# Optimization experiments

Measured on AMD Instinct MI355X. Metric: run time of the kernel, lower is better.

Reference implementation:

```python
import jax, jax.numpy as jnp
import numpy as np

N_JOINTS = 24

def _rodrigues(r):
    # r: [B, J, 3] axis-angle -> [B, J, 3, 3] rotation matrices
    theta = jnp.clip(jnp.linalg.norm(r, axis=-1, keepdims=True), 1e-6)  # [B,J,1]
    rh = r / theta
    z = jnp.zeros_like(rh[..., :1])
    # skew-symmetric matrix m
    m = jnp.stack([
        jnp.concatenate([z, -rh[..., 2:3], rh[..., 1:2]], -1),
        jnp.concatenate([rh[..., 2:3], z, -rh[..., 0:1]], -1),
        jnp.concatenate([-rh[..., 1:2], rh[..., 0:1], z], -1),
    ], axis=-2)  # [B,J,3,3]
    rrT = rh[..., :, None] * rh[..., None, :]  # outer product [B,J,3,3]
    cos = jnp.cos(theta)[..., None]
    sin = jnp.sin(theta)[..., None]
    eye = jnp.eye(3, dtype=r.dtype)
    return cos * eye + (1.0 - cos) * rrT + sin * m

def _with_zeros(Rm, t):
    # Rm: [B,3,3], t: [B,3] -> [B,4,4] homogeneous transform
    B = Rm.shape[0]
    top = jnp.concatenate([Rm, t[:, :, None]], axis=-1)  # [B,3,4]
    bot = jnp.broadcast_to(jnp.array([0.0, 0.0, 0.0, 1.0], Rm.dtype), (B, 1, 4))
    return jnp.concatenate([top, bot], axis=1)

def _keypoints(v, idx):
    # v: [B,N,3], idx: [G,K] vertex-index groups -> [B,G,3] via (max+min)/2
    g = v[:, idx]  # [B,G,K,3] irregular gather
    return (g.max(axis=2) + g.min(axis=2)) * 0.5

def setup_inputs() -> dict:
    key = jax.random.key(0)
    ks = jax.random.split(key, 8)
    B, N, P, K = 64, 40000, 100, 128
    beta = jax.random.normal(ks[0], (B, P), jnp.float32)
    pose = jax.random.normal(ks[1], (B, N_JOINTS * 3), jnp.float32) * 0.3
    trans = jax.random.normal(ks[2], (B, 3), jnp.float32)
    shapedirs = jax.random.normal(ks[3], (P, 3 * N), jnp.float32) * 0.01
    v_template = jax.random.normal(ks[4], (N, 3), jnp.float32)
    w = jax.random.uniform(ks[5], (N, N_JOINTS), jnp.float32)
    weights = w / w.sum(axis=1, keepdims=True)  # LBS weights sum to 1
    reorder_index = jnp.arange(N_JOINTS, dtype=jnp.int64 if jax.config.jax_enable_x64 else jnp.int32)
    # kinematic tree: parent[i] < i (binary-tree shape stands in for the rabbit skeleton)
    parent = jnp.concatenate([jnp.zeros(1, jnp.int32), (jnp.arange(1, N_JOINTS, dtype=jnp.int32) - 1) // 2])
    joint_idx = jax.random.randint(ks[6], (N_JOINTS - 1, K), 0, N)
    add_idx = jax.random.randint(ks[7], (7, K), 0, N)
    return {"beta": beta, "pose": pose, "trans": trans, "shapedirs": shapedirs,
            "v_template": v_template, "weights": weights, "reorder_index": reorder_index,
            "parent": parent, "joint_idx": joint_idx, "add_idx": add_idx}

def reference(beta, pose, trans, shapedirs, v_template, weights,
              reorder_index, parent, joint_idx, add_idx):
    B = beta.shape[0]
    pose = pose.reshape(B, N_JOINTS, 3)[:, reorder_index]
    # blend shapes: v_shaped = beta @ shapedirs + template
    v_posed = (beta @ shapedirs + v_template.reshape(-1)).reshape(B, -1, 3)  # [B,N,3]
    # joints from vertex-group (max+min)/2, root is zero
    J = jnp.concatenate([jnp.zeros((B, 1, 3), beta.dtype), _keypoints(v_posed, joint_idx)], axis=1)  # [B,24,3]
    R = _rodrigues(pose)  # [B,24,3,3]
    # forward kinematics along the tree (fixed 24-joint loop)
    par = np.asarray(jax.device_get(parent))
    G = [_with_zeros(R[:, 0], J[:, 0])]
    for i in range(1, N_JOINTS):
        p = int(par[i])
        G_loc = _with_zeros(R[:, i], J[:, i] - J[:, p])
        G.append(jnp.matmul(G[p], G_loc))
    G = jnp.stack(G, axis=1)  # [B,24,4,4]
    # remove rest-pose joint locations (pack subtraction only touches last column)
    Jh = jnp.concatenate([J, jnp.zeros((B, N_JOINTS, 1), beta.dtype)], axis=-1)[..., None]  # [B,24,4,1]
    t_corr = jnp.matmul(G, Jh)  # [B,24,4,1]
    G1 = jnp.concatenate([G[..., :3], G[..., 3:4] - t_corr], axis=-1)
    # LBS skinning: per-vertex blended transform
    T = jnp.einsum('nk,bkij->bnij', weights, G1)  # [B,N,4,4]
    vh = jnp.concatenate([v_posed, jnp.ones((B, v_posed.shape[1], 1), beta.dtype)], axis=-1)  # [B,N,4]
    posed = jnp.einsum('bnij,bnj->bni', T, vh)[..., :3] + trans[:, None, :]  # [B,N,3]
    skeleton = jnp.concatenate([
        jnp.zeros((B, 1, 3), beta.dtype),
        _keypoints(posed, joint_idx),
        _keypoints(posed, add_idx),
    ], axis=1)  # [B,31,3]
    return posed, skeleton
```

## Files before the change

kernel.cpp:

```cpp
#include <hip/hip_runtime.h>
#include <math.h>

#define B   64
#define NV  40000
#define P   100
#define KG  128
#define NJ  24
#define TV  16
#define NSK 31
#define NSUB (KG / TV)

typedef __attribute__((ext_vector_type(8))) short bf16x8;
typedef __attribute__((ext_vector_type(4))) float f32x4;

__device__ __forceinline__ unsigned short rne_bf16(float f) {
  unsigned u = __float_as_uint(f);
  u = (u + 0x7FFFu + ((u >> 16) & 1u)) >> 16;
  return (unsigned short)u;
}

__global__ __launch_bounds__(256)
void k_jpart(const float* __restrict__ beta,
             const float* __restrict__ sd,
             const float* __restrict__ vt,
             const int*   __restrict__ joint_idx,
             float*       __restrict__ pmn,
             float*       __restrict__ pmx,
             unsigned short* __restrict__ beta_bf) {
  const int j = blockIdx.x;
  const int s = blockIdx.y;
  const int t = threadIdx.x;
  const int lane = t & 63, wv = t >> 6;
  const int l15 = lane & 15, qd = lane >> 4;

  __shared__ __align__(16) unsigned short sdT_s[48 * 136];
  __shared__ __align__(16) float pos_s[64 * 68];
  __shared__ float vt_s[48];
  __shared__ int   idx_s[TV];

  if (t < TV) idx_s[t] = joint_idx[j * KG + s * TV + t];

  if (j == 0 && s == 0) {
    for (int e = t; e < B * 136; e += 256) {
      const int m = e / 136, k = e % 136;
      beta_bf[e] = (k < P) ? rne_bf16(beta[m * P + k]) : (unsigned short)0;
    }
  }
  __syncthreads();

  for (int e = t; e < 48 * 28; e += 256) {
    const int n = e / 28, k = P + e % 28;
    sdT_s[n * 136 + k] = 0;
  }
  for (int task = t; task < TV * P; task += 256) {
    const int v = task / P, k = task % P;
    const float* src = sd + (size_t)k * (3 * NV) + (size_t)idx_s[v] * 3;
    const float f0 = src[0], f1 = src[1], f2 = src[2];
    sdT_s[(v * 3 + 0) * 136 + k] = rne_bf16(f0);
    sdT_s[(v * 3 + 1) * 136 + k] = rne_bf16(f1);
    sdT_s[(v * 3 + 2) * 136 + k] = rne_bf16(f2);
  }
  if (t < 48) vt_s[t] = vt[(size_t)idx_s[t / 3] * 3 + (t % 3)];
  __syncthreads();

  const int m0 = wv * 16 + l15;
  bf16x8 af[4];
#pragma unroll
  for (int ks = 0; ks < 4; ++ks) {
#pragma unroll
    for (int jj = 0; jj < 8; ++jj) {
      const int k = ks * 32 + qd * 8 + jj;
      af[ks][jj] = (short)((k < P) ? rne_bf16(beta[m0 * P + k]) : (unsigned short)0);
    }
  }

  f32x4 acc[3];
#pragma unroll
  for (int nt = 0; nt < 3; ++nt) acc[nt] = (f32x4){0.f, 0.f, 0.f, 0.f};
#pragma unroll
  for (int ks = 0; ks < 4; ++ks) {
#pragma unroll
    for (int nt = 0; nt < 3; ++nt) {
      const bf16x8 bf = *(const bf16x8*)&sdT_s[(nt * 16 + l15) * 136 + ks * 32 + qd * 8];
      acc[nt] = __builtin_amdgcn_mfma_f32_16x16x32_bf16(af[ks], bf, acc[nt], 0, 0, 0);
    }
  }
  float vtv[3];
#pragma unroll
  for (int nt = 0; nt < 3; ++nt) vtv[nt] = vt_s[nt * 16 + l15];

#pragma unroll
  for (int nt = 0; nt < 3; ++nt) {
    const int n = nt * 16 + l15;
    const int v = n / 3, c = n - 3 * v;
#pragma unroll
    for (int r = 0; r < 4; ++r) {
      const int m = wv * 16 + qd * 4 + r;
      pos_s[m * 68 + v * 4 + c] = acc[nt][r] + vtv[nt];
    }
  }
  __syncthreads();

  if (t < 192) {
    const int b = t / 3, c = t % 3;
    float lo = 1e30f, hi = -1e30f;
#pragma unroll
    for (int v = 0; v < TV; ++v) {
      const float val = pos_s[b * 68 + v * 4 + c];
      lo = fminf(lo, val); hi = fmaxf(hi, val);
    }
    pmn[((j * NSUB + s) * B + b) * 3 + c] = lo;
    pmx[((j * NSUB + s) * B + b) * 3 + c] = hi;
  }
}

__global__ void k_chain(const float* __restrict__ pose,
                        const int*   __restrict__ parent,
                        const float* __restrict__ pmn,
                        const float* __restrict__ pmx,
                        const float* __restrict__ trans,
                        unsigned short* __restrict__ G1A) {
  const int b = blockIdx.x;
  const int t = threadIdx.x;

  __shared__ float R[NJ][9];
  __shared__ float Jl[NJ][3];
  __shared__ float G[NJ][12];
  __shared__ float G1c[NJ][12];

  if (t < NJ) {
    const float x = pose[b * NJ * 3 + t * 3 + 0];
    const float y = pose[b * NJ * 3 + t * 3 + 1];
    const float z = pose[b * NJ * 3 + t * 3 + 2];
    const float th = fmaxf(sqrtf(x * x + y * y + z * z), 1e-6f);
    const float xh = x / th, yh = y / th, zh = z / th;
    const float c = cosf(th), s = sinf(th), o = 1.0f - c;
    R[t][0] = c + o * xh * xh;      R[t][1] = o * xh * yh - s * zh; R[t][2] = o * xh * zh + s * yh;
    R[t][3] = o * xh * yh + s * zh; R[t][4] = c + o * yh * yh;      R[t][5] = o * yh * zh - s * xh;
    R[t][6] = o * xh * zh - s * yh; R[t][7] = o * yh * zh + s * xh; R[t][8] = c + o * zh * zh;
    if (t == 0) {
      Jl[0][0] = 0.0f; Jl[0][1] = 0.0f; Jl[0][2] = 0.0f;
    } else {
      const int jj = t - 1;
#pragma unroll
      for (int c2 = 0; c2 < 3; ++c2) {
        float lo = 1e30f, hi = -1e30f;
#pragma unroll
        for (int s2 = 0; s2 < NSUB; ++s2) {
          lo = fminf(lo, pmn[((jj * NSUB + s2) * B + b) * 3 + c2]);
          hi = fmaxf(hi, pmx[((jj * NSUB + s2) * B + b) * 3 + c2]);
        }
        Jl[t][c2] = 0.5f * (lo + hi);
      }
    }
  }
  __syncthreads();

  if (t < 12) {
    const int r = t >> 2, c = t & 3;
    G[0][t] = (c < 3) ? R[0][r * 3 + c] : Jl[0][r];
  }
  __syncthreads();

  for (int i = 1; i < NJ; ++i) {
    const int p = parent[i];
    if (t < 12) {
      const int r = t >> 2, c = t & 3;
      const float g0 = G[p][r * 4 + 0];
      const float g1 = G[p][r * 4 + 1];
      const float g2 = G[p][r * 4 + 2];
      float l0, l1, l2, add;
      if (c < 3) {
        l0 = R[i][0 * 3 + c]; l1 = R[i][1 * 3 + c]; l2 = R[i][2 * 3 + c];
        add = 0.0f;
      } else {
        l0 = Jl[i][0] - Jl[p][0]; l1 = Jl[i][1] - Jl[p][1]; l2 = Jl[i][2] - Jl[p][2];
        add = G[p][r * 4 + 3];
      }
      G[i][t] = g0 * l0 + g1 * l1 + g2 * l2 + add;
    }
    __syncthreads();
  }

  for (int e = t; e < NJ * 12; e += 64) {
    const int i = e / 12, rc = e % 12, r = rc >> 2, c = rc & 3;
    float val;
    if (c < 3) {
      val = G[i][rc];
    } else {
      val = G[i][r * 4 + 3] - (G[i][r * 4 + 0] * Jl[i][0] +
                               G[i][r * 4 + 1] * Jl[i][1] +
                               G[i][r * 4 + 2] * Jl[i][2]);
    }
    G1c[i][rc] = val;
  }
  __syncthreads();

  for (int e = t; e < 512; e += 64) {
    const int m = e >> 5, k = e & 31;
    float val = 0.0f;
    if (m < 12) {
      if (k < NJ) val = G1c[k][m];
      else if (k == NJ && (m & 3) == 3) val = trans[b * 3 + (m >> 2)];
    }
    G1A[(size_t)b * 512 + e] = rne_bf16(val);
  }
}

__global__ __launch_bounds__(256)
void k_skin(const float* __restrict__ sd,
            const float* __restrict__ vt,
            const float* __restrict__ w,
            const unsigned short* __restrict__ beta_bf,
            const unsigned short* __restrict__ G1A,
            float*       __restrict__ out) {
  const int n0v = blockIdx.x * TV;
  const int col0 = n0v * 3;
  const int t  = threadIdx.x;
  const int lane = t & 63, wv = t >> 6;
  const int l15 = lane & 15, q = lane >> 4;

  __shared__ __align__(16) unsigned short sdT_s[48 * 136];
  __shared__ __align__(16) float vhf[64 * 68];

  for (int task = t; task < 768; task += 256) {
    const int n = task % 48, kg = task / 48;
    unsigned pk[4];
#pragma unroll
    for (int h = 0; h < 4; ++h) {
      const int k0 = kg * 8 + 2 * h;
      float f0 = 0.0f, f1 = 0.0f;
      if (k0 < P)     f0 = sd[(size_t)k0 * (3 * NV) + col0 + n];
      if (k0 + 1 < P) f1 = sd[(size_t)(k0 + 1) * (3 * NV) + col0 + n];
      pk[h] = (unsigned)rne_bf16(f0) | ((unsigned)rne_bf16(f1) << 16);
    }
    *(uint4*)&sdT_s[n * 136 + kg * 8] = make_uint4(pk[0], pk[1], pk[2], pk[3]);
  }
  __syncthreads();

  f32x4 acc[3];
#pragma unroll
  for (int nt = 0; nt < 3; ++nt) acc[nt] = (f32x4){0.f, 0.f, 0.f, 0.f};
#pragma unroll
  for (int ks = 0; ks < 4; ++ks) {
    const bf16x8 af = *(const bf16x8*)&beta_bf[(wv * 16 + l15) * 136 + ks * 32 + q * 8];
#pragma unroll
    for (int nt = 0; nt < 3; ++nt) {
      const bf16x8 bf = *(const bf16x8*)&sdT_s[(nt * 16 + l15) * 136 + ks * 32 + q * 8];
      acc[nt] = __builtin_amdgcn_mfma_f32_16x16x32_bf16(af, bf, acc[nt], 0, 0, 0);
    }
  }
  float vtv[3];
#pragma unroll
  for (int nt = 0; nt < 3; ++nt) vtv[nt] = vt[col0 + nt * 16 + l15];

#pragma unroll
  for (int nt = 0; nt < 3; ++nt) {
    const int n = nt * 16 + l15;
    const int v = n / 3, c = n - 3 * v;
#pragma unroll
    for (int r = 0; r < 4; ++r) {
      const int m = wv * 16 + q * 4 + r;
      vhf[m * 68 + v * 4 + c] = acc[nt][r] + vtv[nt];
    }
  }
  __syncthreads();

  bf16x8 wf;
  if (q < 3) {
    const float* wrow = &w[(size_t)(n0v + l15) * NJ + q * 8];
    const float4 w0 = *(const float4*)wrow;
    const float4 w1 = *(const float4*)(wrow + 4);
    wf[0] = (short)rne_bf16(w0.x); wf[1] = (short)rne_bf16(w0.y);
    wf[2] = (short)rne_bf16(w0.z); wf[3] = (short)rne_bf16(w0.w);
    wf[4] = (short)rne_bf16(w1.x); wf[5] = (short)rne_bf16(w1.y);
    wf[6] = (short)rne_bf16(w1.z); wf[7] = (short)rne_bf16(w1.w);
  } else {
    wf = (bf16x8){0, 0, 0, 0, 0, 0, 0, 0};
    wf[0] = (short)0x3F80;
  }
  const f32x4 zero = (f32x4){0.f, 0.f, 0.f, 0.f};
#pragma unroll 4
  for (int bi = 0; bi < 16; ++bi) {
    const int b = wv * 16 + bi;
    const bf16x8 gf = *(const bf16x8*)&G1A[(size_t)b * 512 + l15 * 32 + q * 8];
    const f32x4 d = __builtin_amdgcn_mfma_f32_16x16x32_bf16(gf, wf, zero, 0, 0, 0);
    const float4 vh = *(const float4*)&vhf[b * 68 + l15 * 4];
    if (q < 3) {
      out[(size_t)b * (NV * 3) + col0 + l15 * 3 + q] =
          d[0] * vh.x + d[1] * vh.y + d[2] * vh.z + d[3];
    }
  }
}

__global__ void k_skel(const float* __restrict__ posed,
                       const int*   __restrict__ joint_idx,
                       const int*   __restrict__ add_idx,
                       float*       __restrict__ skel) {
  const int j = blockIdx.x;
  const int b = blockIdx.y;
  const int t = threadIdx.x;
  const int idx = (j < 23) ? joint_idx[j * KG + t] : add_idx[(j - 23) * KG + t];

  const float* p = posed + (size_t)b * NV * 3 + (size_t)idx * 3;
  float mn[3], mx[3];
#pragma unroll
  for (int c = 0; c < 3; ++c) { mn[c] = p[c]; mx[c] = p[c]; }
#pragma unroll
  for (int off = 32; off > 0; off >>= 1) {
#pragma unroll
    for (int c = 0; c < 3; ++c) {
      mn[c] = fminf(mn[c], __shfl_down(mn[c], off));
      mx[c] = fmaxf(mx[c], __shfl_down(mx[c], off));
    }
  }
  __shared__ float s_mn[2][3], s_mx[2][3];
  const int wave = t >> 6, lane = t & 63;
  if (lane == 0) {
#pragma unroll
    for (int c = 0; c < 3; ++c) { s_mn[wave][c] = mn[c]; s_mx[wave][c] = mx[c]; }
  }
  __syncthreads();
  if (t == 0) {
#pragma unroll
    for (int c = 0; c < 3; ++c) {
      float lo = fminf(s_mn[0][c], s_mn[1][c]);
      float hi = fmaxf(s_mx[0][c], s_mx[1][c]);
      skel[(b * NSK + 1 + j) * 3 + c] = 0.5f * (lo + hi);
      if (j == 0) skel[(b * NSK + 0) * 3 + c] = 0.0f;
    }
  }
}

extern "C" void kernel_launch(void* const* d_in, const int* in_sizes, int n_in,
                              void* d_out, int out_size, void* d_ws, size_t ws_size,
                              hipStream_t stream) {
  const float* beta     = (const float*)d_in[0];
  const float* pose     = (const float*)d_in[1];
  const float* trans    = (const float*)d_in[2];
  const float* sd       = (const float*)d_in[3];
  const float* vt       = (const float*)d_in[4];
  const float* w        = (const float*)d_in[5];
  const int* parent     = (const int*)d_in[7];
  const int* joint_idx  = (const int*)d_in[8];
  const int* add_idx    = (const int*)d_in[9];

  float* out = (float*)d_out;
  unsigned short* G1A     = (unsigned short*)d_ws;
  unsigned short* beta_bf = G1A + B * 512;
  float* pmn = (float*)(beta_bf + B * 136);
  float* pmx = pmn + 23 * NSUB * B * 3;

  k_jpart<<<dim3(23, NSUB), 256, 0, stream>>>(beta, sd, vt, joint_idx,
                                              pmn, pmx, beta_bf);
  k_chain<<<B, 64, 0, stream>>>(pose, parent, pmn, pmx, trans, G1A);
  k_skin <<<NV / TV, 256, 0, stream>>>(sd, vt, w, beta_bf, G1A, out);
  k_skel <<<dim3(30, B), 128, 0, stream>>>(out, joint_idx, add_idx,
                                           out + (size_t)B * NV * 3);
}
```

Baseline: 160.7 us.

## Compute skeleton keypoints from gathered vertices instead of re-reading posed output

The skeleton keypoints are now computed by re-skinning only the gathered keypoint vertices, reusing the v_posed tiles that k_jpart already produces (k_jpart now also covers the add_idx groups). The old k_skel kernel did scattered reads of the full posed output after skinning. Beta bf16 conversion moves into a separate prep kernel so k_jpart reads the converted values. This adds two small kernels, extra workspace traffic for the v_posed tiles and more launches, in exchange for removing the dependent scattered gather pass after k_skin.

```diff
diff --git a/kernel.cpp b/kernel.cpp
--- a/kernel.cpp
+++ b/kernel.cpp
@@ -9,6 +9,8 @@
 #define TV  16
 #define NSK 31
 #define NSUB (KG / TV)
+#define NROW 30
+#define VPT  (64 * 68)
 
 typedef __attribute__((ext_vector_type(8))) short bf16x8;
 typedef __attribute__((ext_vector_type(4))) float f32x4;
@@ -19,14 +21,24 @@
   return (unsigned short)u;
 }
 
+__global__ void k_prep(const float* __restrict__ beta,
+                       unsigned short* __restrict__ beta_bf) {
+  const int t = blockIdx.x * 256 + threadIdx.x;
+  if (t < B * 136) {
+    const int m = t / 136, k = t % 136;
+    beta_bf[t] = (k < P) ? rne_bf16(beta[m * P + k]) : (unsigned short)0;
+  }
+}
+
 __global__ __launch_bounds__(256)
-void k_jpart(const float* __restrict__ beta,
+void k_jpart(const unsigned short* __restrict__ beta_bf,
              const float* __restrict__ sd,
              const float* __restrict__ vt,
              const int*   __restrict__ joint_idx,
+             const int*   __restrict__ add_idx,
              float*       __restrict__ pmn,
              float*       __restrict__ pmx,
-             unsigned short* __restrict__ beta_bf) {
+             float*       __restrict__ vposed) {
   const int j = blockIdx.x;
   const int s = blockIdx.y;
   const int t = threadIdx.x;
@@ -38,14 +50,9 @@
   __shared__ float vt_s[48];
   __shared__ int   idx_s[TV];
 
-  if (t < TV) idx_s[t] = joint_idx[j * KG + s * TV + t];
-
-  if (j == 0 && s == 0) {
-    for (int e = t; e < B * 136; e += 256) {
-      const int m = e / 136, k = e % 136;
-      beta_bf[e] = (k < P) ? rne_bf16(beta[m * P + k]) : (unsigned short)0;
-    }
-  }
+  if (t < TV)
+    idx_s[t] = (j < 23) ? joint_idx[j * KG + s * TV + t]
+                        : add_idx[(j - 23) * KG + s * TV + t];
   __syncthreads();
 
   for (int e = t; e < 48 * 28; e += 256) {
@@ -63,26 +70,16 @@
   if (t < 48) vt_s[t] = vt[(size_t)idx_s[t / 3] * 3 + (t % 3)];
   __syncthreads();
 
-  const int m0 = wv * 16 + l15;
-  bf16x8 af[4];
+  f32x4 acc[3];
+#pragma unroll
+  for (int nt = 0; nt < 3; ++nt) acc[nt] = (f32x4){0.f, 0.f, 0.f, 0.f};
 #pragma unroll
   for (int ks = 0; ks < 4; ++ks) {
-#pragma unroll
-    for (int jj = 0; jj < 8; ++jj) {
-      const int k = ks * 32 + qd * 8 + jj;
-      af[ks][jj] = (short)((k < P) ? rne_bf16(beta[m0 * P + k]) : (unsigned short)0);
-    }
-  }
-
-  f32x4 acc[3];
-#pragma unroll
-  for (int nt = 0; nt < 3; ++nt) acc[nt] = (f32x4){0.f, 0.f, 0.f, 0.f};
-#pragma unroll
-  for (int ks = 0; ks < 4; ++ks) {
+    const bf16x8 af = *(const bf16x8*)&beta_bf[(wv * 16 + l15) * 136 + ks * 32 + qd * 8];
 #pragma unroll
     for (int nt = 0; nt < 3; ++nt) {
       const bf16x8 bf = *(const bf16x8*)&sdT_s[(nt * 16 + l15) * 136 + ks * 32 + qd * 8];
-      acc[nt] = __builtin_amdgcn_mfma_f32_16x16x32_bf16(af[ks], bf, acc[nt], 0, 0, 0);
+      acc[nt] = __builtin_amdgcn_mfma_f32_16x16x32_bf16(af, bf, acc[nt], 0, 0, 0);
     }
   }
   float vtv[3];
@@ -101,7 +98,13 @@
   }
   __syncthreads();
 
-  if (t < 192) {
+  {
+    float4* dst = (float4*)(vposed + (size_t)(j * NSUB + s) * VPT);
+    const float4* srcp = (const float4*)pos_s;
+    for (int e = t; e < VPT / 4; e += 256) dst[e] = srcp[e];
+  }
+
+  if (j < 23 && t < 192) {
     const int b = t / 3, c = t % 3;
     float lo = 1e30f, hi = -1e30f;
 #pragma unroll
@@ -208,6 +211,91 @@
 }
 
 __global__ __launch_bounds__(256)
+void k_skel2(const float* __restrict__ vposed,
+             const float* __restrict__ w,
+             const int*   __restrict__ joint_idx,
+             const int*   __restrict__ add_idx,
+             const unsigned short* __restrict__ G1A,
+             float*       __restrict__ pmn2,
+             float*       __restrict__ pmx2) {
+  const int j = blockIdx.x;
+  const int s = blockIdx.y;
+  const int t = threadIdx.x;
+  const int lane = t & 63, wv = t >> 6;
+  const int l15 = lane & 15, q = lane >> 4;
+
+  __shared__ __align__(16) float vhf[64 * 68];
+  __shared__ __align__(16) float pos_s[64 * 68];
+  __shared__ int idx_s[TV];
+
+  if (t < TV)
+    idx_s[t] = (j < 23) ? joint_idx[j * KG + s * TV + t]
+                        : add_idx[(j - 23) * KG + s * TV + t];
+  {
+    const float4* srcp = (const float4*)(vposed + (size_t)(j * NSUB + s) * VPT);
+    float4* dst = (float4*)vhf;
+    for (int e = t; e < VPT / 4; e += 256) dst[e] = srcp[e];
+  }
+  __syncthreads();
+
+  bf16x8 wf;
+  if (q < 3) {
+    const float* wrow = &w[(size_t)idx_s[l15] * NJ + q * 8];
+    const float4 w0 = *(const float4*)wrow;
+    const float4 w1 = *(const float4*)(wrow + 4);
+    wf[0] = (short)rne_bf16(w0.x); wf[1] = (short)rne_bf16(w0.y);
+    wf[2] = (short)rne_bf16(w0.z); wf[3] = (short)rne_bf16(w0.w);
+    wf[4] = (short)rne_bf16(w1.x); wf[5] = (short)rne_bf16(w1.y);
+    wf[6] = (short)rne_bf16(w1.z); wf[7] = (short)rne_bf16(w1.w);
+  } else {
+    wf = (bf16x8){0, 0, 0, 0, 0, 0, 0, 0};
+    wf[0] = (short)0x3F80;
+  }
+  const f32x4 zero = (f32x4){0.f, 0.f, 0.f, 0.f};
+#pragma unroll 4
+  for (int bi = 0; bi < 16; ++bi) {
+    const int b = wv * 16 + bi;
+    const bf16x8 gf = *(const bf16x8*)&G1A[(size_t)b * 512 + l15 * 32 + q * 8];
+    const f32x4 d = __builtin_amdgcn_mfma_f32_16x16x32_bf16(gf, wf, zero, 0, 0, 0);
+    const float4 vh = *(const float4*)&vhf[b * 68 + l15 * 4];
+    if (q < 3) {
+      pos_s[b * 68 + l15 * 4 + q] =
+          d[0] * vh.x + d[1] * vh.y + d[2] * vh.z + d[3];
+    }
+  }
+  __syncthreads();
+
+  if (t < 192) {
+    const int b = t / 3, c = t % 3;
+    float lo = 1e30f, hi = -1e30f;
+#pragma unroll
+    for (int v = 0; v < TV; ++v) {
+      const float val = pos_s[b * 68 + v * 4 + c];
+      lo = fminf(lo, val); hi = fmaxf(hi, val);
+    }
+    pmn2[((j * NSUB + s) * B + b) * 3 + c] = lo;
+    pmx2[((j * NSUB + s) * B + b) * 3 + c] = hi;
+  }
+}
+
+__global__ void k_skelfin(const float* __restrict__ pmn2,
+                          const float* __restrict__ pmx2,
+                          float*       __restrict__ skel) {
+  const int tg = blockIdx.x * 192 + threadIdx.x;
+  const int j = tg / (B * 3);
+  const int rem = tg % (B * 3);
+  const int b = rem / 3, c = rem % 3;
+  float lo = 1e30f, hi = -1e30f;
+#pragma unroll
+  for (int s = 0; s < NSUB; ++s) {
+    lo = fminf(lo, pmn2[((j * NSUB + s) * B + b) * 3 + c]);
+    hi = fmaxf(hi, pmx2[((j * NSUB + s) * B + b) * 3 + c]);
+  }
+  skel[(b * NSK + 1 + j) * 3 + c] = 0.5f * (lo + hi);
+  if (j == 0) skel[(b * NSK + 0) * 3 + c] = 0.0f;
+}
+
+__global__ __launch_bounds__(256)
 void k_skin(const float* __restrict__ sd,
             const float* __restrict__ vt,
             const float* __restrict__ w,
@@ -293,45 +381,6 @@
   }
 }
 
-__global__ void k_skel(const float* __restrict__ posed,
-                       const int*   __restrict__ joint_idx,
-                       const int*   __restrict__ add_idx,
-                       float*       __restrict__ skel) {
-  const int j = blockIdx.x;
-  const int b = blockIdx.y;
-  const int t = threadIdx.x;
-  const int idx = (j < 23) ? joint_idx[j * KG + t] : add_idx[(j - 23) * KG + t];
-
-  const float* p = posed + (size_t)b * NV * 3 + (size_t)idx * 3;
-  float mn[3], mx[3];
-#pragma unroll
-  for (int c = 0; c < 3; ++c) { mn[c] = p[c]; mx[c] = p[c]; }
-#pragma unroll
-  for (int off = 32; off > 0; off >>= 1) {
-#pragma unroll
-    for (int c = 0; c < 3; ++c) {
-      mn[c] = fminf(mn[c], __shfl_down(mn[c], off));
-      mx[c] = fmaxf(mx[c], __shfl_down(mx[c], off));
-    }
-  }
-  __shared__ float s_mn[2][3], s_mx[2][3];
-  const int wave = t >> 6, lane = t & 63;
-  if (lane == 0) {
-#pragma unroll
-    for (int c = 0; c < 3; ++c) { s_mn[wave][c] = mn[c]; s_mx[wave][c] = mx[c]; }
-  }
-  __syncthreads();
-  if (t == 0) {
-#pragma unroll
-    for (int c = 0; c < 3; ++c) {
-      float lo = fminf(s_mn[0][c], s_mn[1][c]);
-      float hi = fmaxf(s_mx[0][c], s_mx[1][c]);
-      skel[(b * NSK + 1 + j) * 3 + c] = 0.5f * (lo + hi);
-      if (j == 0) skel[(b * NSK + 0) * 3 + c] = 0.0f;
-    }
-  }
-}
-
 extern "C" void kernel_launch(void* const* d_in, const int* in_sizes, int n_in,
                               void* d_out, int out_size, void* d_ws, size_t ws_size,
                               hipStream_t stream) {
@@ -348,13 +397,18 @@
   float* out = (float*)d_out;
   unsigned short* G1A     = (unsigned short*)d_ws;
   unsigned short* beta_bf = G1A + B * 512;
-  float* pmn = (float*)(beta_bf + B * 136);
-  float* pmx = pmn + 23 * NSUB * B * 3;
-
-  k_jpart<<<dim3(23, NSUB), 256, 0, stream>>>(beta, sd, vt, joint_idx,
-                                              pmn, pmx, beta_bf);
-  k_chain<<<B, 64, 0, stream>>>(pose, parent, pmn, pmx, trans, G1A);
-  k_skin <<<NV / TV, 256, 0, stream>>>(sd, vt, w, beta_bf, G1A, out);
-  k_skel <<<dim3(30, B), 128, 0, stream>>>(out, joint_idx, add_idx,
-                                           out + (size_t)B * NV * 3);
-}
+  float* pmn    = (float*)(beta_bf + B * 136);
+  float* pmx    = pmn + 23 * NSUB * B * 3;
+  float* pmn2   = pmx + 23 * NSUB * B * 3;
+  float* pmx2   = pmn2 + NROW * NSUB * B * 3;
+  float* vposed = pmx2 + NROW * NSUB * B * 3;
+
+  k_prep  <<<(B * 136 + 255) / 256, 256, 0, stream>>>(beta, beta_bf);
+  k_jpart <<<dim3(NROW, NSUB), 256, 0, stream>>>(beta_bf, sd, vt, joint_idx,
+                                                 add_idx, pmn, pmx, vposed);
+  k_chain <<<B, 64, 0, stream>>>(pose, parent, pmn, pmx, trans, G1A);
+  k_skel2 <<<dim3(NROW, NSUB), 256, 0, stream>>>(vposed, w, joint_idx, add_idx,
+                                                 G1A, pmn2, pmx2);
+  k_skelfin<<<NROW, 192, 0, stream>>>(pmn2, pmx2, out + (size_t)B * NV * 3);
+  k_skin  <<<NV / TV, 256, 0, stream>>>(sd, vt, w, beta_bf, G1A, out);
+}
```

Result: no change. 158.2 us (-1.6%).
